# Kernel tuning notes

Measured on AMD Instinct MI355X. Metric: run time of the kernel, lower is better.

## Reference

```python
import jax, jax.numpy as jnp
import numpy as np

IN_C = 256
HID_C = 256
HEADS = 8
SCALE = 1.0 / np.sqrt(HID_C / HEADS).astype(np.float32)


def setup_inputs() -> dict:
    key = jax.random.key(0)
    k_v, k_q, k_k, k_w, k_o, k_b = jax.random.split(key, 6)
    B, S = 4, 2048
    lim_in = 1.0 / np.sqrt(IN_C)
    lim_out = 1.0 / np.sqrt(IN_C * HEADS)
    v = jax.random.normal(k_v, (B, S, IN_C), dtype=jnp.float32)
    WQ = jax.random.uniform(k_q, (IN_C, IN_C * HEADS), jnp.float32, -lim_in, lim_in)
    WK = jax.random.uniform(k_k, (IN_C, IN_C * HEADS), jnp.float32, -lim_in, lim_in)
    WV = jax.random.uniform(k_w, (IN_C, IN_C * HEADS), jnp.float32, -lim_in, lim_in)
    Wout = jax.random.uniform(k_o, (IN_C * HEADS, HID_C), jnp.float32, -lim_out, lim_out)
    bout = jax.random.uniform(k_b, (HID_C,), jnp.float32, -lim_out, lim_out)
    return {"v": v, "WQ": WQ, "WK": WK, "WV": WV, "Wout": Wout, "bout": bout}


def reference(v, WQ, WK, WV, Wout, bout):
    B, S, C = v.shape  # C == IN_C
    H = HEADS
    # projections, reshape to [b, s, h, c] (per-head dim == in_channels)
    q = (v @ WQ).reshape(B, S, H, C)
    k = (v @ WK).reshape(B, S, H, C)
    val = (v @ WV).reshape(B, S, H, C)
    # scores [b, s1, s2, h]; softmax over s2 (axis=-2 of this layout)
    scores = jnp.einsum('bshc,bthc->bsth', q, k) * SCALE
    A = jax.nn.softmax(scores, axis=2)
    u = jnp.einsum('bsth,bthc->bshc', A, val).reshape(B, S, H * C)
    return u @ Wout + bout
```

## Files before the change

### kernel.cpp

```cpp
#include <hip/hip_runtime.h>
#include <hip/hip_bf16.h>

typedef __bf16 bf16x8 __attribute__((ext_vector_type(8)));
typedef float f32x4 __attribute__((ext_vector_type(4)));
typedef unsigned short ushort8 __attribute__((ext_vector_type(8)));

#define DEVINL static __device__ __forceinline__

DEVINL unsigned f2bf(float f){
  unsigned u = __float_as_uint(f);
  return (u + 0x7fffu + ((u >> 16) & 1u)) >> 16;
}

DEVINL f32x4 MFMA(bf16x8 a, bf16x8 b, f32x4 c){
  return __builtin_amdgcn_mfma_f32_16x16x32_bf16(a, b, c, 0, 0, 0);
}

typedef const __attribute__((address_space(1))) unsigned int* gas_t;
typedef __attribute__((address_space(3))) unsigned int* las_t;
DEVINL void gload_lds16(const void* g, void* l){
  __builtin_amdgcn_global_load_lds((gas_t)g, (las_t)l, 16, 0, 0);
}

DEVINL unsigned cvtpk(float lo, float hi){
  unsigned r; asm("v_cvt_pk_bf16_f32 %0, %1, %2" : "=v"(r) : "v"(lo), "v"(hi)); return r;
}
DEVINL void sw32(unsigned &a, unsigned &b){ asm("v_permlane32_swap_b32 %0, %1" : "+v"(a), "+v"(b)); }
DEVINL void sw16(unsigned &a, unsigned &b){ asm("v_permlane16_swap_b32 %0, %1" : "+v"(a), "+v"(b)); }

__global__ void k_cvt(const float* __restrict__ s, unsigned short* __restrict__ d, int n){
  int i = (blockIdx.x * blockDim.x + threadIdx.x) * 4;
  if (i >= n) return;
  float4 v = *(const float4*)(s + i);
  ushort4 o;
  o.x = (unsigned short)f2bf(v.x); o.y = (unsigned short)f2bf(v.y);
  o.z = (unsigned short)f2bf(v.z); o.w = (unsigned short)f2bf(v.w);
  *(ushort4*)(d + i) = o;
}

__global__ void k_tr4(const float* __restrict__ WQ, const float* __restrict__ WK,
                      const float* __restrict__ WV, const float* __restrict__ Wout,
                      unsigned short* __restrict__ wT, unsigned short* __restrict__ woT){
  __shared__ float t[32][33];
  int id = blockIdx.x;
  const float* s; unsigned short* d; int R, C, tile;
  if (id < 1536){
    int z = id >> 9; tile = id & 511;
    s = (z == 0) ? WQ : ((z == 1) ? WK : WV);
    d = wT + z * 524288; R = 256; C = 2048;
  } else {
    tile = id - 1536; s = Wout; d = woT; R = 2048; C = 256;
  }
  int tilesX = C >> 5;
  int c0 = (tile % tilesX) * 32, r0 = (tile / tilesX) * 32;
  int tx = threadIdx.x, ty = threadIdx.y;
  #pragma unroll
  for (int k2 = 0; k2 < 4; k2++) t[ty + 8*k2][tx] = s[(r0 + ty + 8*k2) * C + c0 + tx];
  __syncthreads();
  #pragma unroll
  for (int k2 = 0; k2 < 4; k2++) d[(c0 + ty + 8*k2) * R + r0 + tx] = (unsigned short)f2bf(t[tx][ty + 8*k2]);
}

__global__ __launch_bounds__(256, 2) void k_qkv(const unsigned short* __restrict__ vb,
    const unsigned short* __restrict__ wT,
    unsigned short* __restrict__ qo, unsigned short* __restrict__ ko, unsigned short* __restrict__ vTo){
  __shared__ unsigned short As[128 * 72];
  __shared__ unsigned short Bs[128 * 72];
  int tid = threadIdx.x;
  int lane = tid & 63, wid = tid >> 6;
  int lr = lane & 15, lg = lane >> 4;
  int wm = (wid >> 1) * 64, wn = (wid & 1) * 64;
  int bn = blockIdx.x, bm = blockIdx.y, z = blockIdx.z;

  const unsigned short* Ag = vb + (bm * 128) * 256;
  const unsigned short* Bg = wT + z * (2048 * 256) + (bn * 128) * 256;

  f32x4 acc[4][4] = {};
  for (int kt = 0; kt < 4; kt++){
    ushort8 ra[4], rb[4];
    #pragma unroll
    for (int p = 0; p < 4; p++){
      int idx = p * 256 + tid; int row = idx >> 3, ch = idx & 7;
      ra[p] = *(const ushort8*)(Ag + row * 256 + kt * 64 + ch * 8);
      rb[p] = *(const ushort8*)(Bg + row * 256 + kt * 64 + ch * 8);
    }
    __syncthreads();
    #pragma unroll
    for (int p = 0; p < 4; p++){
      int idx = p * 256 + tid; int row = idx >> 3, ch = idx & 7;
      *(ushort8*)(As + row * 72 + ch * 8) = ra[p];
      *(ushort8*)(Bs + row * 72 + ch * 8) = rb[p];
    }
    __syncthreads();
    #pragma unroll
    for (int kf = 0; kf < 2; kf++){
      bf16x8 af[4], bfr[4];
      #pragma unroll
      for (int mf = 0; mf < 4; mf++) af[mf]  = *(const bf16x8*)(As + (wm + mf*16 + lr) * 72 + kf*32 + lg*8);
      #pragma unroll
      for (int nf = 0; nf < 4; nf++) bfr[nf] = *(const bf16x8*)(Bs + (wn + nf*16 + lr) * 72 + kf*32 + lg*8);
      #pragma unroll
      for (int mf = 0; mf < 4; mf++)
        #pragma unroll
        for (int nf = 0; nf < 4; nf++)
          acc[mf][nf] = MFMA(af[mf], bfr[nf], acc[mf][nf]);
    }
  }
  if (z < 2){
    unsigned short* dst = z ? ko : qo;
    #pragma unroll
    for (int mf = 0; mf < 4; mf++)
      #pragma unroll
      for (int nf = 0; nf < 4; nf++){
        int mg = bm*128 + wm + mf*16 + lg*4;
        int ng = bn*128 + wn + nf*16 + lr;
        #pragma unroll
        for (int r2 = 0; r2 < 4; r2++) dst[(mg + r2) * 2048 + ng] = (unsigned short)f2bf(acc[mf][nf][r2]);
      }
  } else {
    #pragma unroll
    for (int mf = 0; mf < 4; mf++)
      #pragma unroll
      for (int nf = 0; nf < 4; nf++){
        int mg = bm*128 + wm + mf*16 + lg*4;
        int ng = bn*128 + wn + nf*16 + lr;
        int bb = mg >> 11, s = mg & 2047, hh = ng >> 8, cc = ng & 255;
        uint2 w;
        w.x = f2bf(acc[mf][nf][0]) | (f2bf(acc[mf][nf][1]) << 16);
        w.y = f2bf(acc[mf][nf][2]) | (f2bf(acc[mf][nf][3]) << 16);
        *(uint2*)(vTo + (size_t)((bb*8 + hh) * 256 + cc) * 2048 + s) = w;
      }
  }
}

__global__ __launch_bounds__(256, 2) void k_attn(const unsigned short* __restrict__ q,
    const unsigned short* __restrict__ kk, const unsigned short* __restrict__ vT,
    unsigned short* __restrict__ u){
  __shared__ unsigned short Ks[2][8192];
  __shared__ unsigned short Vs[2][8192];
  int tid = threadIdx.x;
  int lane = tid & 63, wid = tid >> 6;
  int lr = lane & 15, lg = lane >> 4;
  int g = (blockIdx.x & 7) * 64 + (blockIdx.x >> 3);
  int bh = g >> 4, qt = g & 15;
  int b = bh >> 3, h = bh & 7;
  int q0 = qt * 128;

  const char* kgB = (const char*)(kk + (size_t)b * 2048 * 2048 + h * 256);
  const char* vgB = (const char*)(vT + (size_t)(b * 8 + h) * 256 * 2048);
  const unsigned short* qg = q + (size_t)(b * 2048 + q0 + wid * 32) * 2048 + h * 256;

  const char* sp[8];
  bool isK = wid < 2;
  long stepB = isK ? 131072 : 64;
  #pragma unroll
  for (int j = 0; j < 8; j++){
    if (isK){
      int c = wid * 512 + j * 64 + lane;
      int row = c >> 5, slot = c & 31;
      sp[j] = kgB + (size_t)row * 4096 + ((slot ^ (row & 7)) * 16);
    } else {
      int c2 = (wid - 2) * 512 + j * 64 + lane;
      int blk = c2 >> 5, ts = (c2 >> 3) & 3, low3 = c2 & 7;
      int crow = blk * 8 + (low3 ^ (ts * 2));
      sp[j] = vgB + (size_t)crow * 4096 + ts * 16;
    }
  }
  int wbase = (wid & 1) * 8192;
  auto stage = [&](int buf){
    char* db = (char*)(isK ? &Ks[buf][0] : &Vs[buf][0]) + wbase;
    #pragma unroll
    for (int j = 0; j < 8; j++){
      gload_lds16(sp[j], db + j * 1024);
      sp[j] += stepB;
    }
  };

  stage(0);

  bf16x8 qreg[2][8];
  #pragma unroll
  for (int qf = 0; qf < 2; qf++)
    #pragma unroll
    for (int kf = 0; kf < 8; kf++)
      qreg[qf][kf] = *(const bf16x8*)(qg + (size_t)(qf * 16 + lr) * 2048 + kf * 32 + lg * 8);

  f32x4 acc[2][16] = {};
  float lpart[2] = {0.f, 0.f};
  const float SC2   = 0.25503510f;
  const float SHIFT = -11.5415603f;

  int xA = (lg ^ (lr & 7)) * 16;
  int vbase = (lr >> 3) * 512 + lg * 128 + (((lr & 7) ^ (lg * 2)) * 16);

  for (int t0 = 0; t0 < 64; t0++){
    int cur = t0 & 1;
    asm volatile("s_waitcnt vmcnt(0)" ::: "memory");
    __builtin_amdgcn_s_barrier();
    if (t0 + 1 < 64) stage(cur ^ 1);
    const char* Kc = (const char*)Ks[cur];
    const char* Vc = (const char*)Vs[cur];

    f32x4 pt[2][2] = {};
    const char* ka0 = Kc + lr * 512 + xA;
    const char* ka1 = Kc + lr * 512 + (xA ^ 64);
    __builtin_amdgcn_s_setprio(1);
    #pragma unroll
    for (int kf2 = 0; kf2 < 4; kf2++){
      bf16x8 kE0 = *(const bf16x8*)(ka0 + kf2 * 128);
      bf16x8 kO0 = *(const bf16x8*)(ka1 + kf2 * 128);
      bf16x8 kE1 = *(const bf16x8*)(ka0 + 8192 + kf2 * 128);
      bf16x8 kO1 = *(const bf16x8*)(ka1 + 8192 + kf2 * 128);
      pt[0][0] = MFMA(kE0, qreg[0][2*kf2],   pt[0][0]);
      pt[0][1] = MFMA(kE0, qreg[1][2*kf2],   pt[0][1]);
      pt[1][0] = MFMA(kE1, qreg[0][2*kf2],   pt[1][0]);
      pt[1][1] = MFMA(kE1, qreg[1][2*kf2],   pt[1][1]);
      pt[0][0] = MFMA(kO0, qreg[0][2*kf2+1], pt[0][0]);
      pt[0][1] = MFMA(kO0, qreg[1][2*kf2+1], pt[0][1]);
      pt[1][0] = MFMA(kO1, qreg[0][2*kf2+1], pt[1][0]);
      pt[1][1] = MFMA(kO1, qreg[1][2*kf2+1], pt[1][1]);
    }
    __builtin_amdgcn_s_setprio(0);

    bf16x8 pa[2];
    #pragma unroll
    for (int qf = 0; qf < 2; qf++){
      float s0 = 0.f, s1 = 0.f;
      #pragma unroll
      for (int tf = 0; tf < 2; tf++)
        #pragma unroll
        for (int r2 = 0; r2 < 4; r2++){
          float e = __builtin_amdgcn_exp2f(fmaf(pt[tf][qf][r2], SC2, SHIFT));
          pt[tf][qf][r2] = e;
          if (r2 & 1) s1 += e; else s0 += e;
        }
      lpart[qf] += s0 + s1;
      unsigned A = cvtpk(pt[0][qf][0], pt[0][qf][1]);
      unsigned B = cvtpk(pt[0][qf][2], pt[0][qf][3]);
      unsigned C = cvtpk(pt[1][qf][0], pt[1][qf][1]);
      unsigned D = cvtpk(pt[1][qf][2], pt[1][qf][3]);
      sw32(A, C); sw32(B, D);
      sw16(A, C); sw16(B, D);
      union { unsigned w[4]; bf16x8 v; } cv;
      cv.w[0] = A; cv.w[1] = B; cv.w[2] = C; cv.w[3] = D;
      pa[qf] = cv.v;
    }

    __builtin_amdgcn_s_setprio(1);
    #pragma unroll
    for (int nf = 0; nf < 16; nf++){
      bf16x8 vf = *(const bf16x8*)(Vc + nf * 1024 + vbase);
      acc[0][nf] = MFMA(pa[0], vf, acc[0][nf]);
      acc[1][nf] = MFMA(pa[1], vf, acc[1][nf]);
    }
    __builtin_amdgcn_s_setprio(0);
  }
  #pragma unroll
  for (int qf = 0; qf < 2; qf++){
    lpart[qf] += __shfl_xor(lpart[qf], 16);
    lpart[qf] += __shfl_xor(lpart[qf], 32);
  }
  #pragma unroll
  for (int mf = 0; mf < 2; mf++){
    float inv = 1.f / lpart[mf];
    float i4[4];
    #pragma unroll
    for (int r2 = 0; r2 < 4; r2++) i4[r2] = __shfl(inv, lg * 4 + r2);
    #pragma unroll
    for (int nf = 0; nf < 16; nf++)
      #pragma unroll
      for (int r2 = 0; r2 < 4; r2++){
        int s = q0 + wid * 32 + mf * 16 + lg * 4 + r2;
        int c = nf * 16 + lr;
        u[(size_t)(b * 2048 + s) * 2048 + h * 256 + c] = (unsigned short)f2bf(acc[mf][nf][r2] * i4[r2]);
      }
  }
}

__global__ __launch_bounds__(256, 2) void k_out(const unsigned short* __restrict__ u,
    const unsigned short* __restrict__ woT, const float* __restrict__ bout, float* __restrict__ out){
  __shared__ unsigned short As[64 * 72];
  __shared__ unsigned short Bs[64 * 72];
  int tid = threadIdx.x;
  int lane = tid & 63, wid = tid >> 6;
  int lr = lane & 15, lg = lane >> 4;
  int wm = (wid >> 1) * 32, wn = (wid & 1) * 32;
  int bn = blockIdx.x, bm = blockIdx.y;
  const unsigned short* Ag = u + (size_t)(bm * 64) * 2048;
  const unsigned short* Bg = woT + (size_t)(bn * 64) * 2048;
  f32x4 acc[2][2] = {};
  for (int kt = 0; kt < 32; kt++){
    ushort8 ra[2], rb[2];
    #pragma unroll
    for (int p = 0; p < 2; p++){
      int idx = p * 256 + tid; int row = idx >> 3, ch = idx & 7;
      ra[p] = *(const ushort8*)(Ag + (size_t)row * 2048 + kt*64 + ch*8);
      rb[p] = *(const ushort8*)(Bg + (size_t)row * 2048 + kt*64 + ch*8);
    }
    __syncthreads();
    #pragma unroll
    for (int p = 0; p < 2; p++){
      int idx = p * 256 + tid; int row = idx >> 3, ch = idx & 7;
      *(ushort8*)(As + row * 72 + ch * 8) = ra[p];
      *(ushort8*)(Bs + row * 72 + ch * 8) = rb[p];
    }
    __syncthreads();
    #pragma unroll
    for (int kf = 0; kf < 2; kf++){
      bf16x8 a0 = *(const bf16x8*)(As + (wm + lr) * 72      + kf*32 + lg*8);
      bf16x8 a1 = *(const bf16x8*)(As + (wm + 16 + lr) * 72 + kf*32 + lg*8);
      bf16x8 b0 = *(const bf16x8*)(Bs + (wn + lr) * 72      + kf*32 + lg*8);
      bf16x8 b1 = *(const bf16x8*)(Bs + (wn + 16 + lr) * 72 + kf*32 + lg*8);
      acc[0][0] = MFMA(a0, b0, acc[0][0]); acc[0][1] = MFMA(a0, b1, acc[0][1]);
      acc[1][0] = MFMA(a1, b0, acc[1][0]); acc[1][1] = MFMA(a1, b1, acc[1][1]);
    }
  }
  #pragma unroll
  for (int mf = 0; mf < 2; mf++)
    #pragma unroll
    for (int nf = 0; nf < 2; nf++){
      int mg = bm*64 + wm + mf*16 + lg*4;
      int ng = bn*64 + wn + nf*16 + lr;
      #pragma unroll
      for (int r2 = 0; r2 < 4; r2++) out[(size_t)(mg + r2) * 256 + ng] = acc[mf][nf][r2] + bout[ng];
    }
}

extern "C" void kernel_launch(void* const* d_in, const int* in_sizes, int n_in,
                              void* d_out, int out_size, void* d_ws, size_t ws_size,
                              hipStream_t stream){
  const float* v    = (const float*)d_in[0];
  const float* WQ   = (const float*)d_in[1];
  const float* WK   = (const float*)d_in[2];
  const float* WV   = (const float*)d_in[3];
  const float* Wout = (const float*)d_in[4];
  const float* bout = (const float*)d_in[5];
  char* ws = (char*)d_ws;
  unsigned short* vb  = (unsigned short*)(ws);
  unsigned short* wT  = (unsigned short*)(ws + (4u  << 20));
  unsigned short* woT = (unsigned short*)(ws + (7u  << 20));
  unsigned short* qb  = (unsigned short*)(ws + (8u  << 20));
  unsigned short* kb  = (unsigned short*)(ws + (40u << 20));
  unsigned short* vTb = (unsigned short*)(ws + (72u << 20));
  unsigned short* ub  = (unsigned short*)(ws + (104u << 20));
  float* out = (float*)d_out;

  k_cvt<<<2048, 256, 0, stream>>>(v, vb, 2097152);
  k_tr4<<<2048, dim3(32, 8), 0, stream>>>(WQ, WK, WV, Wout, wT, woT);
  k_qkv<<<dim3(16, 64, 3), 256, 0, stream>>>(vb, wT, qb, kb, vTb);
  k_attn<<<512, 256, 0, stream>>>(qb, kb, vTb, ub);
  k_out<<<dim3(4, 128), 256, 0, stream>>>(ub, woT, bout, out);
}
```

Before: 207.2 us.

## Pre-pack K into MFMA fragment layout and fold softmax scale into WQ

The QKV projection now writes K in a tiled layout that matches the MFMA operand fragments. The attention kernel reads K fragments straight from global memory into registers, so it no longer stages K through LDS and only V is double-buffered. The softmax scale is folded into WQ during weight transposition, and the constant exp2 shift is dropped, which removes an FMA per score. The cost is that each wave now loads K from global memory with no prefetch, so every wave re-reads the same tile and that latency sits inside the MFMA loop. The K epilogue also switches to scattered 2-byte stores.

```diff
diff --git a/kernel.cpp b/kernel.cpp
--- a/kernel.cpp
+++ b/kernel.cpp
@@ -44,9 +44,11 @@
   __shared__ float t[32][33];
   int id = blockIdx.x;
   const float* s; unsigned short* d; int R, C, tile;
+  float scl = 1.0f;
   if (id < 1536){
     int z = id >> 9; tile = id & 511;
     s = (z == 0) ? WQ : ((z == 1) ? WK : WV);
+    if (z == 0) scl = 0.25503510f;
     d = wT + z * 524288; R = 256; C = 2048;
   } else {
     tile = id - 1536; s = Wout; d = woT; R = 2048; C = 256;
@@ -58,12 +60,12 @@
   for (int k2 = 0; k2 < 4; k2++) t[ty + 8*k2][tx] = s[(r0 + ty + 8*k2) * C + c0 + tx];
   __syncthreads();
   #pragma unroll
-  for (int k2 = 0; k2 < 4; k2++) d[(c0 + ty + 8*k2) * R + r0 + tx] = (unsigned short)f2bf(t[tx][ty + 8*k2]);
+  for (int k2 = 0; k2 < 4; k2++) d[(c0 + ty + 8*k2) * R + r0 + tx] = (unsigned short)f2bf(t[tx][ty + 8*k2] * scl);
 }
 
 __global__ __launch_bounds__(256, 2) void k_qkv(const unsigned short* __restrict__ vb,
     const unsigned short* __restrict__ wT,
-    unsigned short* __restrict__ qo, unsigned short* __restrict__ ko, unsigned short* __restrict__ vTo){
+    unsigned short* __restrict__ qo, char* __restrict__ kpB, unsigned short* __restrict__ vTo){
   __shared__ unsigned short As[128 * 72];
   __shared__ unsigned short Bs[128 * 72];
   int tid = threadIdx.x;
@@ -106,8 +108,7 @@
           acc[mf][nf] = MFMA(af[mf], bfr[nf], acc[mf][nf]);
     }
   }
-  if (z < 2){
-    unsigned short* dst = z ? ko : qo;
+  if (z == 0){
     #pragma unroll
     for (int mf = 0; mf < 4; mf++)
       #pragma unroll
@@ -115,7 +116,23 @@
         int mg = bm*128 + wm + mf*16 + lg*4;
         int ng = bn*128 + wn + nf*16 + lr;
         #pragma unroll
-        for (int r2 = 0; r2 < 4; r2++) dst[(mg + r2) * 2048 + ng] = (unsigned short)f2bf(acc[mf][nf][r2]);
+        for (int r2 = 0; r2 < 4; r2++) qo[(mg + r2) * 2048 + ng] = (unsigned short)f2bf(acc[mf][nf][r2]);
+      }
+  } else if (z == 1){
+    #pragma unroll
+    for (int mf = 0; mf < 4; mf++)
+      #pragma unroll
+      for (int nf = 0; nf < 4; nf++){
+        int mg = bm*128 + wm + mf*16 + lg*4;
+        int ng = bn*128 + wn + nf*16 + lr;
+        int bb = mg >> 11, si = mg & 2047;
+        int hh = ng >> 8, cc = ng & 255;
+        int t0 = si >> 5, trow = si & 31, tf = trow >> 4, lrr = trow & 15;
+        int kfi = cc >> 5, lgg = (cc >> 3) & 3, e = cc & 7;
+        size_t base = ((size_t)(bb*8 + hh) << 20) + t0*16384 + (tf*8 + kfi)*1024 + (lgg*16 + lrr)*16 + e*2;
+        #pragma unroll
+        for (int r2 = 0; r2 < 4; r2++)
+          *(unsigned short*)(kpB + base + r2*16) = (unsigned short)f2bf(acc[mf][nf][r2]);
       }
   } else {
     #pragma unroll
@@ -134,9 +151,8 @@
 }
 
 __global__ __launch_bounds__(256, 2) void k_attn(const unsigned short* __restrict__ q,
-    const unsigned short* __restrict__ kk, const unsigned short* __restrict__ vT,
+    const char* __restrict__ kp, const unsigned short* __restrict__ vT,
     unsigned short* __restrict__ u){
-  __shared__ unsigned short Ks[2][8192];
   __shared__ unsigned short Vs[2][8192];
   int tid = threadIdx.x;
   int lane = tid & 63, wid = tid >> 6;
@@ -146,33 +162,24 @@
   int b = bh >> 3, h = bh & 7;
   int q0 = qt * 128;
 
-  const char* kgB = (const char*)(kk + (size_t)b * 2048 * 2048 + h * 256);
+  const char* kph = kp + ((size_t)(b * 8 + h) << 20);
   const char* vgB = (const char*)(vT + (size_t)(b * 8 + h) * 256 * 2048);
   const unsigned short* qg = q + (size_t)(b * 2048 + q0 + wid * 32) * 2048 + h * 256;
 
-  const char* sp[8];
-  bool isK = wid < 2;
-  long stepB = isK ? 131072 : 64;
-  #pragma unroll
-  for (int j = 0; j < 8; j++){
-    if (isK){
-      int c = wid * 512 + j * 64 + lane;
-      int row = c >> 5, slot = c & 31;
-      sp[j] = kgB + (size_t)row * 4096 + ((slot ^ (row & 7)) * 16);
-    } else {
-      int c2 = (wid - 2) * 512 + j * 64 + lane;
-      int blk = c2 >> 5, ts = (c2 >> 3) & 3, low3 = c2 & 7;
-      int crow = blk * 8 + (low3 ^ (ts * 2));
-      sp[j] = vgB + (size_t)crow * 4096 + ts * 16;
-    }
-  }
-  int wbase = (wid & 1) * 8192;
+  const char* sp[4];
+  #pragma unroll
+  for (int j = 0; j < 4; j++){
+    int c2 = wid * 256 + j * 64 + lane;
+    int blk = c2 >> 5, ts = (c2 >> 3) & 3, low3 = c2 & 7;
+    int crow = blk * 8 + (low3 ^ (ts * 2));
+    sp[j] = vgB + (size_t)crow * 4096 + ts * 16;
+  }
   auto stage = [&](int buf){
-    char* db = (char*)(isK ? &Ks[buf][0] : &Vs[buf][0]) + wbase;
-    #pragma unroll
-    for (int j = 0; j < 8; j++){
+    char* db = (char*)&Vs[buf][0] + wid * 4096;
+    #pragma unroll
+    for (int j = 0; j < 4; j++){
       gload_lds16(sp[j], db + j * 1024);
-      sp[j] += stepB;
+      sp[j] += 64;
     }
   };
 
@@ -187,10 +194,7 @@
 
   f32x4 acc[2][16] = {};
   float lpart[2] = {0.f, 0.f};
-  const float SC2   = 0.25503510f;
-  const float SHIFT = -11.5415603f;
-
-  int xA = (lg ^ (lr & 7)) * 16;
+  int lane16 = lane * 16;
   int vbase = (lr >> 3) * 512 + lg * 128 + (((lr & 7) ^ (lg * 2)) * 16);
 
   for (int t0 = 0; t0 < 64; t0++){
@@ -198,19 +202,16 @@
     asm volatile("s_waitcnt vmcnt(0)" ::: "memory");
     __builtin_amdgcn_s_barrier();
     if (t0 + 1 < 64) stage(cur ^ 1);
-    const char* Kc = (const char*)Ks[cur];
     const char* Vc = (const char*)Vs[cur];
 
     f32x4 pt[2][2] = {};
-    const char* ka0 = Kc + lr * 512 + xA;
-    const char* ka1 = Kc + lr * 512 + (xA ^ 64);
     __builtin_amdgcn_s_setprio(1);
     #pragma unroll
     for (int kf2 = 0; kf2 < 4; kf2++){
-      bf16x8 kE0 = *(const bf16x8*)(ka0 + kf2 * 128);
-      bf16x8 kO0 = *(const bf16x8*)(ka1 + kf2 * 128);
-      bf16x8 kE1 = *(const bf16x8*)(ka0 + 8192 + kf2 * 128);
-      bf16x8 kO1 = *(const bf16x8*)(ka1 + 8192 + kf2 * 128);
+      bf16x8 kE0 = *(const bf16x8*)(kph + (2*kf2    ) * 1024 + lane16);
+      bf16x8 kO0 = *(const bf16x8*)(kph + (2*kf2 + 1) * 1024 + lane16);
+      bf16x8 kE1 = *(const bf16x8*)(kph + (2*kf2 + 8) * 1024 + lane16);
+      bf16x8 kO1 = *(const bf16x8*)(kph + (2*kf2 + 9) * 1024 + lane16);
       pt[0][0] = MFMA(kE0, qreg[0][2*kf2],   pt[0][0]);
       pt[0][1] = MFMA(kE0, qreg[1][2*kf2],   pt[0][1]);
       pt[1][0] = MFMA(kE1, qreg[0][2*kf2],   pt[1][0]);
@@ -230,7 +231,7 @@
       for (int tf = 0; tf < 2; tf++)
         #pragma unroll
         for (int r2 = 0; r2 < 4; r2++){
-          float e = __builtin_amdgcn_exp2f(fmaf(pt[tf][qf][r2], SC2, SHIFT));
+          float e = __builtin_amdgcn_exp2f(pt[tf][qf][r2]);
           pt[tf][qf][r2] = e;
           if (r2 & 1) s1 += e; else s0 += e;
         }
@@ -254,6 +255,7 @@
       acc[1][nf] = MFMA(pa[1], vf, acc[1][nf]);
     }
     __builtin_amdgcn_s_setprio(0);
+    kph += 16384;
   }
   #pragma unroll
   for (int qf = 0; qf < 2; qf++){
@@ -340,14 +342,14 @@
   unsigned short* wT  = (unsigned short*)(ws + (4u  << 20));
   unsigned short* woT = (unsigned short*)(ws + (7u  << 20));
   unsigned short* qb  = (unsigned short*)(ws + (8u  << 20));
-  unsigned short* kb  = (unsigned short*)(ws + (40u << 20));
+  char*           kpB = (char*)          (ws + (40u << 20));
   unsigned short* vTb = (unsigned short*)(ws + (72u << 20));
   unsigned short* ub  = (unsigned short*)(ws + (104u << 20));
   float* out = (float*)d_out;
 
   k_cvt<<<2048, 256, 0, stream>>>(v, vb, 2097152);
   k_tr4<<<2048, dim3(32, 8), 0, stream>>>(WQ, WK, WV, Wout, wT, woT);
-  k_qkv<<<dim3(16, 64, 3), 256, 0, stream>>>(vb, wT, qb, kb, vTb);
-  k_attn<<<512, 256, 0, stream>>>(qb, kb, vTb, ub);
+  k_qkv<<<dim3(16, 64, 3), 256, 0, stream>>>(vb, wT, qb, kpB, vTb);
+  k_attn<<<512, 256, 0, stream>>>(qb, kpB, vTb, ub);
   k_out<<<dim3(4, 128), 256, 0, stream>>>(ub, woT, bout, out);
 }
```

Measured after the change: 312.7 us. 1.51x slower.

## Switch attention kernel to 32x32x16 MFMA tiles and fold softmax scale into WQ

Applied to the files above, without the earlier changes.

Rewrites the attention inner loops to use 32x32x16 bf16 MFMA instead of 16x16x32. This halves the LDS fragment loads per tile and removes one permlane swap stage when repacking probabilities. The softmax scale (log2e/sqrt(d)) is folded into WQ during weight conversion, so the exp2 no longer needs an FMA. The fixed SHIFT offset is dropped. Larger accumulators raise register pressure, and dropping the shift changes numeric range, with a risk of overflow for large scores.

```diff
diff --git a/kernel.cpp b/kernel.cpp
--- a/kernel.cpp
+++ b/kernel.cpp
@@ -3,6 +3,7 @@
 
 typedef __bf16 bf16x8 __attribute__((ext_vector_type(8)));
 typedef float f32x4 __attribute__((ext_vector_type(4)));
+typedef float f32x16 __attribute__((ext_vector_type(16)));
 typedef unsigned short ushort8 __attribute__((ext_vector_type(8)));
 
 #define DEVINL static __device__ __forceinline__
@@ -14,6 +15,9 @@
 
 DEVINL f32x4 MFMA(bf16x8 a, bf16x8 b, f32x4 c){
   return __builtin_amdgcn_mfma_f32_16x16x32_bf16(a, b, c, 0, 0, 0);
+}
+DEVINL f32x16 MFMA32(bf16x8 a, bf16x8 b, f32x16 c){
+  return __builtin_amdgcn_mfma_f32_32x32x16_bf16(a, b, c, 0, 0, 0);
 }
 
 typedef const __attribute__((address_space(1))) unsigned int* gas_t;
@@ -26,7 +30,6 @@
   unsigned r; asm("v_cvt_pk_bf16_f32 %0, %1, %2" : "=v"(r) : "v"(lo), "v"(hi)); return r;
 }
 DEVINL void sw32(unsigned &a, unsigned &b){ asm("v_permlane32_swap_b32 %0, %1" : "+v"(a), "+v"(b)); }
-DEVINL void sw16(unsigned &a, unsigned &b){ asm("v_permlane16_swap_b32 %0, %1" : "+v"(a), "+v"(b)); }
 
 __global__ void k_cvt(const float* __restrict__ s, unsigned short* __restrict__ d, int n){
   int i = (blockIdx.x * blockDim.x + threadIdx.x) * 4;
@@ -44,9 +47,11 @@
   __shared__ float t[32][33];
   int id = blockIdx.x;
   const float* s; unsigned short* d; int R, C, tile;
+  float scl = 1.0f;
   if (id < 1536){
     int z = id >> 9; tile = id & 511;
     s = (z == 0) ? WQ : ((z == 1) ? WK : WV);
+    if (z == 0) scl = 0.25503510f;
     d = wT + z * 524288; R = 256; C = 2048;
   } else {
     tile = id - 1536; s = Wout; d = woT; R = 2048; C = 256;
@@ -58,7 +63,7 @@
   for (int k2 = 0; k2 < 4; k2++) t[ty + 8*k2][tx] = s[(r0 + ty + 8*k2) * C + c0 + tx];
   __syncthreads();
   #pragma unroll
-  for (int k2 = 0; k2 < 4; k2++) d[(c0 + ty + 8*k2) * R + r0 + tx] = (unsigned short)f2bf(t[tx][ty + 8*k2]);
+  for (int k2 = 0; k2 < 4; k2++) d[(c0 + ty + 8*k2) * R + r0 + tx] = (unsigned short)f2bf(t[tx][ty + 8*k2] * scl);
 }
 
 __global__ __launch_bounds__(256, 2) void k_qkv(const unsigned short* __restrict__ vb,
@@ -140,7 +145,7 @@
   __shared__ unsigned short Vs[2][8192];
   int tid = threadIdx.x;
   int lane = tid & 63, wid = tid >> 6;
-  int lr = lane & 15, lg = lane >> 4;
+  int l31 = lane & 31, hi = lane >> 5;
   int g = (blockIdx.x & 7) * 64 + (blockIdx.x >> 3);
   int bh = g >> 4, qt = g & 15;
   int b = bh >> 3, h = bh & 7;
@@ -178,20 +183,18 @@
 
   stage(0);
 
-  bf16x8 qreg[2][8];
-  #pragma unroll
-  for (int qf = 0; qf < 2; qf++)
-    #pragma unroll
-    for (int kf = 0; kf < 8; kf++)
-      qreg[qf][kf] = *(const bf16x8*)(qg + (size_t)(qf * 16 + lr) * 2048 + kf * 32 + lg * 8);
-
-  f32x4 acc[2][16] = {};
-  float lpart[2] = {0.f, 0.f};
-  const float SC2   = 0.25503510f;
-  const float SHIFT = -11.5415603f;
-
-  int xA = (lg ^ (lr & 7)) * 16;
-  int vbase = (lr >> 3) * 512 + lg * 128 + (((lr & 7) ^ (lg * 2)) * 16);
+  bf16x8 qreg[16];
+  #pragma unroll
+  for (int s = 0; s < 16; s++)
+    qreg[s] = *(const bf16x8*)(qg + (size_t)l31 * 2048 + s * 16 + hi * 8);
+
+  f32x16 acc[8] = {};
+  float lpart = 0.f;
+
+  int kb2 = l31 * 512 + ((hi ^ (lane & 1)) << 4);
+  int xh  = (lane >> 1) & 3;
+  int vb0 = (l31 >> 3) * 512 + hi * 128 + (((lane & 7) ^ (2 * hi)) * 16);
+  int vb1 = (l31 >> 3) * 512 + (2 + hi) * 128 + (((lane & 7) ^ (4 + 2 * hi)) * 16);
 
   for (int t0 = 0; t0 < 64; t0++){
     int cur = t0 & 1;
@@ -201,80 +204,62 @@
     const char* Kc = (const char*)Ks[cur];
     const char* Vc = (const char*)Vs[cur];
 
-    f32x4 pt[2][2] = {};
-    const char* ka0 = Kc + lr * 512 + xA;
-    const char* ka1 = Kc + lr * 512 + (xA ^ 64);
+    f32x16 pt = {};
     __builtin_amdgcn_s_setprio(1);
     #pragma unroll
-    for (int kf2 = 0; kf2 < 4; kf2++){
-      bf16x8 kE0 = *(const bf16x8*)(ka0 + kf2 * 128);
-      bf16x8 kO0 = *(const bf16x8*)(ka1 + kf2 * 128);
-      bf16x8 kE1 = *(const bf16x8*)(ka0 + 8192 + kf2 * 128);
-      bf16x8 kO1 = *(const bf16x8*)(ka1 + 8192 + kf2 * 128);
-      pt[0][0] = MFMA(kE0, qreg[0][2*kf2],   pt[0][0]);
-      pt[0][1] = MFMA(kE0, qreg[1][2*kf2],   pt[0][1]);
-      pt[1][0] = MFMA(kE1, qreg[0][2*kf2],   pt[1][0]);
-      pt[1][1] = MFMA(kE1, qreg[1][2*kf2],   pt[1][1]);
-      pt[0][0] = MFMA(kO0, qreg[0][2*kf2+1], pt[0][0]);
-      pt[0][1] = MFMA(kO0, qreg[1][2*kf2+1], pt[0][1]);
-      pt[1][0] = MFMA(kO1, qreg[0][2*kf2+1], pt[1][0]);
-      pt[1][1] = MFMA(kO1, qreg[1][2*kf2+1], pt[1][1]);
+    for (int s = 0; s < 16; s++){
+      bf16x8 ka = *(const bf16x8*)(Kc + kb2 + ((s ^ xh) << 5));
+      pt = MFMA32(ka, qreg[s], pt);
     }
     __builtin_amdgcn_s_setprio(0);
 
-    bf16x8 pa[2];
-    #pragma unroll
-    for (int qf = 0; qf < 2; qf++){
-      float s0 = 0.f, s1 = 0.f;
-      #pragma unroll
-      for (int tf = 0; tf < 2; tf++)
-        #pragma unroll
-        for (int r2 = 0; r2 < 4; r2++){
-          float e = __builtin_amdgcn_exp2f(fmaf(pt[tf][qf][r2], SC2, SHIFT));
-          pt[tf][qf][r2] = e;
-          if (r2 & 1) s1 += e; else s0 += e;
-        }
-      lpart[qf] += s0 + s1;
-      unsigned A = cvtpk(pt[0][qf][0], pt[0][qf][1]);
-      unsigned B = cvtpk(pt[0][qf][2], pt[0][qf][3]);
-      unsigned C = cvtpk(pt[1][qf][0], pt[1][qf][1]);
-      unsigned D = cvtpk(pt[1][qf][2], pt[1][qf][3]);
-      sw32(A, C); sw32(B, D);
-      sw16(A, C); sw16(B, D);
-      union { unsigned w[4]; bf16x8 v; } cv;
-      cv.w[0] = A; cv.w[1] = B; cv.w[2] = C; cv.w[3] = D;
-      pa[qf] = cv.v;
-    }
+    float e[16];
+    float s0 = 0.f, s1 = 0.f;
+    #pragma unroll
+    for (int r = 0; r < 16; r++){
+      float ev = __builtin_amdgcn_exp2f(pt[r]);
+      e[r] = ev;
+      if (r & 1) s1 += ev; else s0 += ev;
+    }
+    lpart += s0 + s1;
+    unsigned w0 = cvtpk(e[0],  e[1]),  w1 = cvtpk(e[2],  e[3]);
+    unsigned w2 = cvtpk(e[4],  e[5]),  w3 = cvtpk(e[6],  e[7]);
+    unsigned w4 = cvtpk(e[8],  e[9]),  w5 = cvtpk(e[10], e[11]);
+    unsigned w6 = cvtpk(e[12], e[13]), w7 = cvtpk(e[14], e[15]);
+    sw32(w0, w2); sw32(w1, w3);
+    sw32(w4, w6); sw32(w5, w7);
+    union { unsigned w[4]; bf16x8 v; } cv0, cv1;
+    cv0.w[0] = w0; cv0.w[1] = w1; cv0.w[2] = w2; cv0.w[3] = w3;
+    cv1.w[0] = w4; cv1.w[1] = w5; cv1.w[2] = w6; cv1.w[3] = w7;
+    bf16x8 pa0 = cv0.v;
+    bf16x8 pa1 = cv1.v;
 
     __builtin_amdgcn_s_setprio(1);
     #pragma unroll
-    for (int nf = 0; nf < 16; nf++){
-      bf16x8 vf = *(const bf16x8*)(Vc + nf * 1024 + vbase);
-      acc[0][nf] = MFMA(pa[0], vf, acc[0][nf]);
-      acc[1][nf] = MFMA(pa[1], vf, acc[1][nf]);
+    for (int nf = 0; nf < 8; nf++){
+      bf16x8 v0 = *(const bf16x8*)(Vc + nf * 2048 + vb0);
+      bf16x8 v1 = *(const bf16x8*)(Vc + nf * 2048 + vb1);
+      acc[nf] = MFMA32(pa0, v0, acc[nf]);
+      acc[nf] = MFMA32(pa1, v1, acc[nf]);
     }
     __builtin_amdgcn_s_setprio(0);
   }
-  #pragma unroll
-  for (int qf = 0; qf < 2; qf++){
-    lpart[qf] += __shfl_xor(lpart[qf], 16);
-    lpart[qf] += __shfl_xor(lpart[qf], 32);
-  }
-  #pragma unroll
-  for (int mf = 0; mf < 2; mf++){
-    float inv = 1.f / lpart[mf];
-    float i4[4];
-    #pragma unroll
-    for (int r2 = 0; r2 < 4; r2++) i4[r2] = __shfl(inv, lg * 4 + r2);
-    #pragma unroll
-    for (int nf = 0; nf < 16; nf++)
-      #pragma unroll
-      for (int r2 = 0; r2 < 4; r2++){
-        int s = q0 + wid * 32 + mf * 16 + lg * 4 + r2;
-        int c = nf * 16 + lr;
-        u[(size_t)(b * 2048 + s) * 2048 + h * 256 + c] = (unsigned short)f2bf(acc[mf][nf][r2] * i4[r2]);
-      }
-  }
+  lpart += __shfl_xor(lpart, 32);
+  float inv = 1.f / lpart;
+  float iv[16];
+  #pragma unroll
+  for (int r = 0; r < 16; r++){
+    int qq = (r & 3) + 8 * (r >> 2) + 4 * hi;
+    iv[r] = __shfl(inv, qq);
+  }
+  unsigned short* ug = u + (size_t)(b * 2048 + q0 + wid * 32) * 2048 + h * 256;
+  #pragma unroll
+  for (int nf = 0; nf < 8; nf++)
+    #pragma unroll
+    for (int r = 0; r < 16; r++){
+      int qq = (r & 3) + 8 * (r >> 2) + 4 * hi;
+      ug[(size_t)qq * 2048 + nf * 32 + l31] = (unsigned short)f2bf(acc[nf][r] * iv[r]);
+    }
 }
 
 __global__ __launch_bounds__(256, 2) void k_out(const unsigned short* __restrict__ u,
```

New measurement: 219.1 us. 5.7% more time.

## Double-buffer GEMM LDS tiles, fold softmax scale into WQ, merge prep kernels

Applied to the files above, without the earlier changes.

The QKV and output-projection GEMMs now use two LDS buffers. The next k-tile's global loads are issued before the barrier and written to the alternate buffer after the MFMAs, which drops one barrier per iteration and overlaps loads with compute. The softmax scale is folded into WQ during the weight transpose, and the constant exp2 shift is dropped, so the attention inner loop does a bare exp2 instead of an fma plus exp2. Without the shift, large scores could overflow before normalization. The input cast and weight-transpose kernels are merged into one launch.

```diff
diff --git a/kernel.cpp b/kernel.cpp
--- a/kernel.cpp
+++ b/kernel.cpp
@@ -28,28 +28,33 @@
 DEVINL void sw32(unsigned &a, unsigned &b){ asm("v_permlane32_swap_b32 %0, %1" : "+v"(a), "+v"(b)); }
 DEVINL void sw16(unsigned &a, unsigned &b){ asm("v_permlane16_swap_b32 %0, %1" : "+v"(a), "+v"(b)); }
 
-__global__ void k_cvt(const float* __restrict__ s, unsigned short* __restrict__ d, int n){
-  int i = (blockIdx.x * blockDim.x + threadIdx.x) * 4;
-  if (i >= n) return;
-  float4 v = *(const float4*)(s + i);
-  ushort4 o;
-  o.x = (unsigned short)f2bf(v.x); o.y = (unsigned short)f2bf(v.y);
-  o.z = (unsigned short)f2bf(v.z); o.w = (unsigned short)f2bf(v.w);
-  *(ushort4*)(d + i) = o;
-}
-
-__global__ void k_tr4(const float* __restrict__ WQ, const float* __restrict__ WK,
-                      const float* __restrict__ WV, const float* __restrict__ Wout,
-                      unsigned short* __restrict__ wT, unsigned short* __restrict__ woT){
+__global__ void k_prep(const float* __restrict__ v, const float* __restrict__ WQ,
+                       const float* __restrict__ WK, const float* __restrict__ WV,
+                       const float* __restrict__ Wout,
+                       unsigned short* __restrict__ vb,
+                       unsigned short* __restrict__ wT, unsigned short* __restrict__ woT){
+  int tid = threadIdx.y * 32 + threadIdx.x;
+  int id = blockIdx.x;
+  if (id < 2048){
+    int i = (id * 256 + tid) * 4;
+    float4 x = *(const float4*)(v + i);
+    ushort4 o;
+    o.x = (unsigned short)f2bf(x.x); o.y = (unsigned short)f2bf(x.y);
+    o.z = (unsigned short)f2bf(x.z); o.w = (unsigned short)f2bf(x.w);
+    *(ushort4*)(vb + i) = o;
+    return;
+  }
   __shared__ float t[32][33];
-  int id = blockIdx.x;
+  int id2 = id - 2048;
   const float* s; unsigned short* d; int R, C, tile;
-  if (id < 1536){
-    int z = id >> 9; tile = id & 511;
+  float scl = 1.0f;
+  if (id2 < 1536){
+    int z = id2 >> 9; tile = id2 & 511;
     s = (z == 0) ? WQ : ((z == 1) ? WK : WV);
+    if (z == 0) scl = 0.25503510f;
     d = wT + z * 524288; R = 256; C = 2048;
   } else {
-    tile = id - 1536; s = Wout; d = woT; R = 2048; C = 256;
+    tile = id2 - 1536; s = Wout; d = woT; R = 2048; C = 256;
   }
   int tilesX = C >> 5;
   int c0 = (tile % tilesX) * 32, r0 = (tile / tilesX) * 32;
@@ -58,14 +63,14 @@
   for (int k2 = 0; k2 < 4; k2++) t[ty + 8*k2][tx] = s[(r0 + ty + 8*k2) * C + c0 + tx];
   __syncthreads();
   #pragma unroll
-  for (int k2 = 0; k2 < 4; k2++) d[(c0 + ty + 8*k2) * R + r0 + tx] = (unsigned short)f2bf(t[tx][ty + 8*k2]);
+  for (int k2 = 0; k2 < 4; k2++) d[(c0 + ty + 8*k2) * R + r0 + tx] = (unsigned short)f2bf(t[tx][ty + 8*k2] * scl);
 }
 
 __global__ __launch_bounds__(256, 2) void k_qkv(const unsigned short* __restrict__ vb,
     const unsigned short* __restrict__ wT,
     unsigned short* __restrict__ qo, unsigned short* __restrict__ ko, unsigned short* __restrict__ vTo){
-  __shared__ unsigned short As[128 * 72];
-  __shared__ unsigned short Bs[128 * 72];
+  __shared__ unsigned short As[2][9216];
+  __shared__ unsigned short Bs[2][9216];
   int tid = threadIdx.x;
   int lane = tid & 63, wid = tid >> 6;
   int lr = lane & 15, lg = lane >> 4;
@@ -75,35 +80,54 @@
   const unsigned short* Ag = vb + (bm * 128) * 256;
   const unsigned short* Bg = wT + z * (2048 * 256) + (bn * 128) * 256;
 
+  ushort8 ra[4], rb[4];
+  #pragma unroll
+  for (int p = 0; p < 4; p++){
+    int idx = p * 256 + tid; int row = idx >> 3, ch = idx & 7;
+    ra[p] = *(const ushort8*)(Ag + row * 256 + ch * 8);
+    rb[p] = *(const ushort8*)(Bg + row * 256 + ch * 8);
+  }
+  #pragma unroll
+  for (int p = 0; p < 4; p++){
+    int idx = p * 256 + tid; int row = idx >> 3, ch = idx & 7;
+    *(ushort8*)(&As[0][row * 72 + ch * 8]) = ra[p];
+    *(ushort8*)(&Bs[0][row * 72 + ch * 8]) = rb[p];
+  }
+
   f32x4 acc[4][4] = {};
+  #pragma unroll
   for (int kt = 0; kt < 4; kt++){
-    ushort8 ra[4], rb[4];
-    #pragma unroll
-    for (int p = 0; p < 4; p++){
-      int idx = p * 256 + tid; int row = idx >> 3, ch = idx & 7;
-      ra[p] = *(const ushort8*)(Ag + row * 256 + kt * 64 + ch * 8);
-      rb[p] = *(const ushort8*)(Bg + row * 256 + kt * 64 + ch * 8);
+    if (kt < 3){
+      #pragma unroll
+      for (int p = 0; p < 4; p++){
+        int idx = p * 256 + tid; int row = idx >> 3, ch = idx & 7;
+        ra[p] = *(const ushort8*)(Ag + row * 256 + (kt + 1) * 64 + ch * 8);
+        rb[p] = *(const ushort8*)(Bg + row * 256 + (kt + 1) * 64 + ch * 8);
+      }
     }
     __syncthreads();
-    #pragma unroll
-    for (int p = 0; p < 4; p++){
-      int idx = p * 256 + tid; int row = idx >> 3, ch = idx & 7;
-      *(ushort8*)(As + row * 72 + ch * 8) = ra[p];
-      *(ushort8*)(Bs + row * 72 + ch * 8) = rb[p];
-    }
-    __syncthreads();
+    const unsigned short* Ac = As[kt & 1];
+    const unsigned short* Bc = Bs[kt & 1];
     #pragma unroll
     for (int kf = 0; kf < 2; kf++){
       bf16x8 af[4], bfr[4];
       #pragma unroll
-      for (int mf = 0; mf < 4; mf++) af[mf]  = *(const bf16x8*)(As + (wm + mf*16 + lr) * 72 + kf*32 + lg*8);
-      #pragma unroll
-      for (int nf = 0; nf < 4; nf++) bfr[nf] = *(const bf16x8*)(Bs + (wn + nf*16 + lr) * 72 + kf*32 + lg*8);
+      for (int mf = 0; mf < 4; mf++) af[mf]  = *(const bf16x8*)(Ac + (wm + mf*16 + lr) * 72 + kf*32 + lg*8);
+      #pragma unroll
+      for (int nf = 0; nf < 4; nf++) bfr[nf] = *(const bf16x8*)(Bc + (wn + nf*16 + lr) * 72 + kf*32 + lg*8);
       #pragma unroll
       for (int mf = 0; mf < 4; mf++)
         #pragma unroll
         for (int nf = 0; nf < 4; nf++)
           acc[mf][nf] = MFMA(af[mf], bfr[nf], acc[mf][nf]);
+    }
+    if (kt < 3){
+      #pragma unroll
+      for (int p = 0; p < 4; p++){
+        int idx = p * 256 + tid; int row = idx >> 3, ch = idx & 7;
+        *(ushort8*)(&As[(kt + 1) & 1][row * 72 + ch * 8]) = ra[p];
+        *(ushort8*)(&Bs[(kt + 1) & 1][row * 72 + ch * 8]) = rb[p];
+      }
     }
   }
   if (z < 2){
@@ -187,8 +211,6 @@
 
   f32x4 acc[2][16] = {};
   float lpart[2] = {0.f, 0.f};
-  const float SC2   = 0.25503510f;
-  const float SHIFT = -11.5415603f;
 
   int xA = (lg ^ (lr & 7)) * 16;
   int vbase = (lr >> 3) * 512 + lg * 128 + (((lr & 7) ^ (lg * 2)) * 16);
@@ -230,7 +252,7 @@
       for (int tf = 0; tf < 2; tf++)
         #pragma unroll
         for (int r2 = 0; r2 < 4; r2++){
-          float e = __builtin_amdgcn_exp2f(fmaf(pt[tf][qf][r2], SC2, SHIFT));
+          float e = __builtin_amdgcn_exp2f(pt[tf][qf][r2]);
           pt[tf][qf][r2] = e;
           if (r2 & 1) s1 += e; else s0 += e;
         }
@@ -279,8 +301,8 @@
 
 __global__ __launch_bounds__(256, 2) void k_out(const unsigned short* __restrict__ u,
     const unsigned short* __restrict__ woT, const float* __restrict__ bout, float* __restrict__ out){
-  __shared__ unsigned short As[64 * 72];
-  __shared__ unsigned short Bs[64 * 72];
+  __shared__ unsigned short As[2][4608];
+  __shared__ unsigned short Bs[2][4608];
   int tid = threadIdx.x;
   int lane = tid & 63, wid = tid >> 6;
   int lr = lane & 15, lg = lane >> 4;
@@ -288,31 +310,50 @@
   int bn = blockIdx.x, bm = blockIdx.y;
   const unsigned short* Ag = u + (size_t)(bm * 64) * 2048;
   const unsigned short* Bg = woT + (size_t)(bn * 64) * 2048;
+
+  ushort8 ra[2], rb[2];
+  #pragma unroll
+  for (int p = 0; p < 2; p++){
+    int idx = p * 256 + tid; int row = idx >> 3, ch = idx & 7;
+    ra[p] = *(const ushort8*)(Ag + (size_t)row * 2048 + ch * 8);
+    rb[p] = *(const ushort8*)(Bg + (size_t)row * 2048 + ch * 8);
+  }
+  #pragma unroll
+  for (int p = 0; p < 2; p++){
+    int idx = p * 256 + tid; int row = idx >> 3, ch = idx & 7;
+    *(ushort8*)(&As[0][row * 72 + ch * 8]) = ra[p];
+    *(ushort8*)(&Bs[0][row * 72 + ch * 8]) = rb[p];
+  }
+
   f32x4 acc[2][2] = {};
   for (int kt = 0; kt < 32; kt++){
-    ushort8 ra[2], rb[2];
-    #pragma unroll
-    for (int p = 0; p < 2; p++){
-      int idx = p * 256 + tid; int row = idx >> 3, ch = idx & 7;
-      ra[p] = *(const ushort8*)(Ag + (size_t)row * 2048 + kt*64 + ch*8);
-      rb[p] = *(const ushort8*)(Bg + (size_t)row * 2048 + kt*64 + ch*8);
+    if (kt < 31){
+      #pragma unroll
+      for (int p = 0; p < 2; p++){
+        int idx = p * 256 + tid; int row = idx >> 3, ch = idx & 7;
+        ra[p] = *(const ushort8*)(Ag + (size_t)row * 2048 + (kt + 1) * 64 + ch * 8);
+        rb[p] = *(const ushort8*)(Bg + (size_t)row * 2048 + (kt + 1) * 64 + ch * 8);
+      }
     }
     __syncthreads();
-    #pragma unroll
-    for (int p = 0; p < 2; p++){
-      int idx = p * 256 + tid; int row = idx >> 3, ch = idx & 7;
-      *(ushort8*)(As + row * 72 + ch * 8) = ra[p];
-      *(ushort8*)(Bs + row * 72 + ch * 8) = rb[p];
-    }
-    __syncthreads();
+    const unsigned short* Ac = As[kt & 1];
+    const unsigned short* Bc = Bs[kt & 1];
     #pragma unroll
     for (int kf = 0; kf < 2; kf++){
-      bf16x8 a0 = *(const bf16x8*)(As + (wm + lr) * 72      + kf*32 + lg*8);
-      bf16x8 a1 = *(const bf16x8*)(As + (wm + 16 + lr) * 72 + kf*32 + lg*8);
-      bf16x8 b0 = *(const bf16x8*)(Bs + (wn + lr) * 72      + kf*32 + lg*8);
-      bf16x8 b1 = *(const bf16x8*)(Bs + (wn + 16 + lr) * 72 + kf*32 + lg*8);
+      bf16x8 a0 = *(const bf16x8*)(Ac + (wm + lr) * 72      + kf*32 + lg*8);
+      bf16x8 a1 = *(const bf16x8*)(Ac + (wm + 16 + lr) * 72 + kf*32 + lg*8);
+      bf16x8 b0 = *(const bf16x8*)(Bc + (wn + lr) * 72      + kf*32 + lg*8);
+      bf16x8 b1 = *(const bf16x8*)(Bc + (wn + 16 + lr) * 72 + kf*32 + lg*8);
       acc[0][0] = MFMA(a0, b0, acc[0][0]); acc[0][1] = MFMA(a0, b1, acc[0][1]);
       acc[1][0] = MFMA(a1, b0, acc[1][0]); acc[1][1] = MFMA(a1, b1, acc[1][1]);
+    }
+    if (kt < 31){
+      #pragma unroll
+      for (int p = 0; p < 2; p++){
+        int idx = p * 256 + tid; int row = idx >> 3, ch = idx & 7;
+        *(ushort8*)(&As[(kt + 1) & 1][row * 72 + ch * 8]) = ra[p];
+        *(ushort8*)(&Bs[(kt + 1) & 1][row * 72 + ch * 8]) = rb[p];
+      }
     }
   }
   #pragma unroll
@@ -345,8 +386,7 @@
   unsigned short* ub  = (unsigned short*)(ws + (104u << 20));
   float* out = (float*)d_out;
 
-  k_cvt<<<2048, 256, 0, stream>>>(v, vb, 2097152);
-  k_tr4<<<2048, dim3(32, 8), 0, stream>>>(WQ, WK, WV, Wout, wT, woT);
+  k_prep<<<4096, dim3(32, 8), 0, stream>>>(v, WQ, WK, WV, Wout, vb, wT, woT);
   k_qkv<<<dim3(16, 64, 3), 256, 0, stream>>>(vb, wT, qb, kb, vTb);
   k_attn<<<512, 256, 0, stream>>>(qb, kb, vTb, ub);
   k_out<<<dim3(4, 128), 256, 0, stream>>>(ub, woT, bout, out);
```

Result: faster. 201.2 us (-2.9%).
